# Kernel tuning notes

Measured on AMD Instinct MI355X. Metric: run time of the kernel, lower is better.

Reference implementation:

```python
import jax, jax.numpy as jnp
import numpy as np
from jax import lax

SIGMAS = (15.0, 80.0, 250.0)
DETAIL_WEIGHT = 0.0
ILLUM_WEIGHT = 1.0
EPS = 0.001


def _gaussian_kernel1d(sigma: float) -> np.ndarray:
    ks = int(2 * round(3 * sigma) + 1)
    if ks % 2 == 0:
        ks += 1
    x = np.arange(ks, dtype=np.float32) - (ks - 1) / 2.0
    k = np.exp(-0.5 * (x / sigma) ** 2)
    return (k / k.sum()).astype(np.float32)


def _gaussian_blur(img: jnp.ndarray, sigma: float) -> jnp.ndarray:
    # Separable Gaussian blur with reflect padding (kornia gaussian_blur2d semantics).
    k = jnp.asarray(_gaussian_kernel1d(sigma))
    ks = k.shape[0]
    p = ks // 2
    C = img.shape[1]
    dn = ('NCHW', 'OIHW', 'NCHW')
    kv = jnp.broadcast_to(k.reshape(1, 1, ks, 1), (C, 1, ks, 1))  # vertical pass
    kh = jnp.broadcast_to(k.reshape(1, 1, 1, ks), (C, 1, 1, ks))  # horizontal pass
    x = jnp.pad(img, ((0, 0), (0, 0), (p, p), (0, 0)), mode='reflect')
    x = lax.conv_general_dilated(x, kv, (1, 1), 'VALID', dimension_numbers=dn,
                                 feature_group_count=C)
    x = jnp.pad(x, ((0, 0), (0, 0), (0, 0), (p, p)), mode='reflect')
    x = lax.conv_general_dilated(x, kh, (1, 1), 'VALID', dimension_numbers=dn,
                                 feature_group_count=C)
    return x


def _multi_scale_retinex(input_img: jnp.ndarray) -> jnp.ndarray:
    img = jnp.clip(input_img, EPS, 1.0)
    log_img = jnp.log(img)
    acc = jnp.zeros_like(log_img)
    for sigma in SIGMAS:
        blur = jnp.maximum(_gaussian_blur(img, sigma), EPS)
        acc = acc + (log_img - jnp.log(blur))
    return acc / len(SIGMAS)


def setup_inputs() -> dict:
    key = jax.random.key(0)
    input_img = jax.random.uniform(key, (2, 3, 1024, 1024), dtype=jnp.float32)
    return {"input_img": input_img}


def reference(input_img):
    reflectance = _multi_scale_retinex(input_img)
    gx = reflectance[:, :, :, :-1] - reflectance[:, :, :, 1:]
    gy = reflectance[:, :, :-1, :] - reflectance[:, :, 1:, :]
    loss_detail = jnp.abs(gx).mean() + jnp.abs(gy).mean()
    illumination = jnp.log(jnp.maximum(input_img, EPS)) - reflectance
    igx = illumination[:, :, :, :-1] - illumination[:, :, :, 1:]
    igy = illumination[:, :, :-1, :] - illumination[:, :, 1:, :]
    loss_smooth_illum = jnp.abs(igx).mean() + jnp.abs(igy).mean()
    loss = DETAIL_WEIGHT * loss_detail + ILLUM_WEIGHT * loss_smooth_illum
    return (loss, loss_detail, loss_smooth_illum, reflectance, illumination)
```

## Files before the change

### kernel.cpp

```cpp
#include <hip/hip_runtime.h>
#include <math.h>

#define IMN 1024
#define IMGSZ (IMN * IMN)
#define NIMG 6
#define EPSV 0.001f
#define NB1 4096

typedef unsigned short u16;
typedef _Float16 f16;
typedef __attribute__((ext_vector_type(8))) _Float16 half8;
typedef __attribute__((ext_vector_type(16))) float floatx16;

__device__ __forceinline__ u16 f16_bits(float v) {
  union { f16 h; u16 b; } u;
  u.h = (f16)v;
  return u.b;
}

__global__ __launch_bounds__(256) void build_taps_k(float* __restrict__ taps) {
  const int kss[3] = {91, 481, 1501};
  const float sig[3] = {15.f, 80.f, 250.f};
  int s = blockIdx.x;
  int ks = kss[s];
  float sigma = sig[s];
  float* t = taps + s * 1536;
  float ctr = (float)(ks - 1) * 0.5f;
  __shared__ float red[256];
  float loc = 0.f;
  for (int i = threadIdx.x; i < ks; i += 256) {
    float x = ((float)i - ctr) / sigma;
    float v = expf(-0.5f * x * x);
    t[i] = v;
    loc += v;
  }
  red[threadIdx.x] = loc;
  __syncthreads();
  for (int o = 128; o > 0; o >>= 1) {
    if (threadIdx.x < o) red[threadIdx.x] += red[threadIdx.x + o];
    __syncthreads();
  }
  float inv = 1.f / red[0];
  for (int i = threadIdx.x; i < ks; i += 256) t[i] *= inv;
}

__global__ __launch_bounds__(256) void build_w_k(const float* __restrict__ taps, int ks,
                                                 u16* __restrict__ WFr) {
  int r = blockIdx.x;
  int p = ks >> 1;
  __shared__ float row[IMN];
  for (int i = threadIdx.x; i < IMN; i += 256) row[i] = 0.f;
  __syncthreads();
  for (int t = threadIdx.x; t < ks; t += 256) {
    int q = r + t - p;
    int j = q < 0 ? -q : (q > IMN - 1 ? 2 * (IMN - 1) - q : q);
    atomicAdd(&row[j], taps[t]);
  }
  __syncthreads();
  for (int i = threadIdx.x; i < IMN; i += 256)
    WFr[r * IMN + i] = f16_bits(row[i] * 256.f);
}

__global__ __launch_bounds__(256) void split_img_k(const float* __restrict__ inp,
                                                   u16* __restrict__ H) {
  int i4 = (blockIdx.x * 256 + threadIdx.x) * 4;
  float4 v = *(const float4*)&inp[i4];
  float x[4] = {v.x, v.y, v.z, v.w};
  u16 h[4];
#pragma unroll
  for (int e = 0; e < 4; e++) h[e] = f16_bits(fminf(fmaxf(x[e], EPSV), 1.f));
  *(uint2*)&H[i4] = make_uint2((unsigned)h[0] | ((unsigned)h[1] << 16),
                               (unsigned)h[2] | ((unsigned)h[3] << 16));
}

template <int EPI>
__global__ __launch_bounds__(256, 4) void gemm_pass(
    const u16* __restrict__ AH, const u16* __restrict__ WF,
    u16* __restrict__ OH, float* __restrict__ OF, int sBase, int outByZ, int rmw) {
  __shared__ u16 smem[2 * 128 * 32 + 256];
  u16* Af = smem;
  u16* Bf = smem + 128 * 32;
  int z = blockIdx.z;
  int zs = z / 6;
  int s = (gridDim.z >= 18) ? (sBase + 2 - zs) : (sBase + zs);
  int i = z - zs * 6;
  const u16* Ag = AH + (size_t)(EPI == 0 ? i : z) * IMGSZ;
  const u16* Bg = WF + (size_t)s * IMGSZ;
  int bm = blockIdx.y * 128, bn = blockIdx.x * 128;
  int tid = threadIdx.x;
  int lane = tid & 63, w = tid >> 6;
  int wm = (w >> 1) * 64, wn = (w & 1) * 64;
  int lrow = lane & 31, lh = lane >> 5;
  int sig = (lrow >> 1) & 3;
  int tr = tid >> 2;
  int tc = (tid & 3) * 8;
  int sslot = ((tid & 3) ^ ((tr >> 1) & 3)) * 8;
  floatx16 acc[2][2] = {};

  int p = (s == 0) ? 45 : (s == 1) ? 240 : 750;
  int klo = bn - p;
  klo = (klo < 0 ? 0 : klo) & ~31;
  int khi = bn + 128 + p;
  if (khi > IMN) khi = IMN;

  for (int k0 = klo; k0 < khi; k0 += 32) {
    uint4 a0 = *(const uint4*)&Ag[(size_t)(bm + tr) * IMN + k0 + tc];
    uint4 a1 = *(const uint4*)&Ag[(size_t)(bm + tr + 64) * IMN + k0 + tc];
    uint4 b0 = *(const uint4*)&Bg[(size_t)(bn + tr) * IMN + k0 + tc];
    uint4 b1 = *(const uint4*)&Bg[(size_t)(bn + tr + 64) * IMN + k0 + tc];
    *(uint4*)&Af[tr * 32 + sslot] = a0;
    *(uint4*)&Af[(tr + 64) * 32 + sslot] = a1;
    *(uint4*)&Bf[tr * 32 + sslot] = b0;
    *(uint4*)&Bf[(tr + 64) * 32 + sslot] = b1;
    __syncthreads();
#pragma unroll
    for (int kk = 0; kk < 32; kk += 16) {
      int sl = (kk >> 3) + lh;
      int so = ((sl ^ sig) * 8);
      half8 ah[2], bh[2];
#pragma unroll
      for (int mt = 0; mt < 2; mt++)
        ah[mt] = *(const half8*)&Af[(wm + mt * 32 + lrow) * 32 + so];
#pragma unroll
      for (int nt2 = 0; nt2 < 2; nt2++)
        bh[nt2] = *(const half8*)&Bf[(wn + nt2 * 32 + lrow) * 32 + so];
#pragma unroll
      for (int mt = 0; mt < 2; mt++)
#pragma unroll
        for (int nt2 = 0; nt2 < 2; nt2++)
          acc[mt][nt2] = __builtin_amdgcn_mfma_f32_32x32x16_f16(ah[mt], bh[nt2], acc[mt][nt2], 0, 0, 0);
    }
    __syncthreads();
  }

  float* lf = (float*)smem + w * 1056;
#pragma unroll
  for (int mt = 0; mt < 2; mt++)
#pragma unroll
    for (int nt = 0; nt < 2; nt++) {
#pragma unroll
      for (int rq = 0; rq < 4; rq++)
#pragma unroll
        for (int e = 0; e < 4; e++)
          lf[lrow * 33 + rq * 8 + lh * 4 + e] = acc[mt][nt][rq * 4 + e];
      __syncthreads();
#pragma unroll
      for (int p4 = 0; p4 < 4; p4++) {
        int rl = p4 * 8 + (lane >> 3);
        int cl = (lane & 7) * 4;
        float v0 = lf[rl * 33 + cl + 0];
        float v1 = lf[rl * 33 + cl + 1];
        float v2 = lf[rl * 33 + cl + 2];
        float v3 = lf[rl * 33 + cl + 3];
        int gn = bn + wn + nt * 32 + rl;
        int gm = bm + wm + mt * 32 + cl;
        if (EPI == 0) {
          size_t go = (size_t)z * IMGSZ + (size_t)gn * IMN + gm;
          *(uint2*)&OH[go] = make_uint2(
              (unsigned)f16_bits(v0) | ((unsigned)f16_bits(v1) << 16),
              (unsigned)f16_bits(v2) | ((unsigned)f16_bits(v3) << 16));
        } else {
          const float us = 0x1p-16f;
          size_t go = (size_t)(outByZ ? z : i) * IMGSZ + (size_t)gn * IMN + gm;
          float4 rr = make_float4(logf(fmaxf(v0 * us, EPSV)), logf(fmaxf(v1 * us, EPSV)),
                                  logf(fmaxf(v2 * us, EPSV)), logf(fmaxf(v3 * us, EPSV)));
          if (rmw) {
            float4 pa = *(const float4*)&OF[go];
            rr.x += pa.x; rr.y += pa.y; rr.z += pa.z; rr.w += pa.w;
          }
          *(float4*)&OF[go] = rr;
        }
      }
      __syncthreads();
    }
}

__global__ __launch_bounds__(256) void loss_stage1_k(const float* __restrict__ inp,
                                                     const float* __restrict__ lb, int three,
                                                     float* __restrict__ refl,
                                                     float* __restrict__ illum,
                                                     float* __restrict__ pd,
                                                     float* __restrict__ ps) {
  const int stride = NB1 * 256;
  const int S = NIMG * IMGSZ;
  float sd = 0.f, ss = 0.f;
  for (int i = blockIdx.x * 256 + threadIdx.x; i < S; i += stride) {
    int c = i & (IMN - 1);
    int rr = (i >> 10) & (IMN - 1);
    float a0 = lb[i];
    if (three) a0 += lb[i + S] + lb[i + 2 * S];
    float I0 = a0 * (1.f / 3.f);
    float R0 = logf(fmaxf(inp[i], EPSV)) - I0;
    refl[i] = R0;
    illum[i] = I0;
    if (c < IMN - 1) {
      float a1 = lb[i + 1];
      if (three) a1 += lb[i + 1 + S] + lb[i + 1 + 2 * S];
      float I1 = a1 * (1.f / 3.f);
      float R1 = logf(fmaxf(inp[i + 1], EPSV)) - I1;
      sd += fabsf(R0 - R1);
      ss += fabsf(I0 - I1);
    }
    if (rr < IMN - 1) {
      float a2 = lb[i + IMN];
      if (three) a2 += lb[i + IMN + S] + lb[i + IMN + 2 * S];
      float I2 = a2 * (1.f / 3.f);
      float R2 = logf(fmaxf(inp[i + IMN], EPSV)) - I2;
      sd += fabsf(R0 - R2);
      ss += fabsf(I0 - I2);
    }
  }
  for (int o = 32; o > 0; o >>= 1) {
    sd += __shfl_down(sd, o);
    ss += __shfl_down(ss, o);
  }
  __shared__ float rsd[4], rss[4];
  int lane = threadIdx.x & 63, w = threadIdx.x >> 6;
  if (lane == 0) { rsd[w] = sd; rss[w] = ss; }
  __syncthreads();
  if (threadIdx.x == 0) {
    pd[blockIdx.x] = rsd[0] + rsd[1] + rsd[2] + rsd[3];
    ps[blockIdx.x] = rss[0] + rss[1] + rss[2] + rss[3];
  }
}

__global__ __launch_bounds__(256) void loss_stage2_k(const float* __restrict__ pd,
                                                     const float* __restrict__ ps,
                                                     float* __restrict__ out) {
  float sd = 0.f, ss = 0.f;
  for (int i = threadIdx.x; i < NB1; i += 256) {
    sd += pd[i];
    ss += ps[i];
  }
  for (int o = 32; o > 0; o >>= 1) {
    sd += __shfl_down(sd, o);
    ss += __shfl_down(ss, o);
  }
  __shared__ float rsd[4], rss[4];
  int lane = threadIdx.x & 63, w = threadIdx.x >> 6;
  if (lane == 0) { rsd[w] = sd; rss[w] = ss; }
  __syncthreads();
  if (threadIdx.x == 0) {
    float tsd = rsd[0] + rsd[1] + rsd[2] + rsd[3];
    float tss = rss[0] + rss[1] + rss[2] + rss[3];
    const float sc = 1.f / 6285312.f;
    out[0] = tss * sc;
    out[1] = tsd * sc;
    out[2] = tss * sc;
  }
}

extern "C" void kernel_launch(void* const* d_in, const int* in_sizes, int n_in,
                              void* d_out, int out_size, void* d_ws, size_t ws_size,
                              hipStream_t stream) {
  const float* inp = (const float*)d_in[0];
  float* out = (float*)d_out;
  float* refl = out + 3;
  float* illum = refl + (size_t)NIMG * IMGSZ;
  const int kss[3] = {91, 481, 1501};

  char* p = (char*)d_ws;
  float* taps = (float*)p;                  p += 32768;
  u16* WF = (u16*)p;                        p += (size_t)3 * IMGSZ * 2;
  u16* imgF = (u16*)p;                      p += (size_t)NIMG * IMGSZ * 2;
  size_t fixed = (size_t)(p - (char*)d_ws);
  size_t needT1 = fixed + (size_t)18 * IMGSZ * 2 + (size_t)18 * IMGSZ * 4;
  bool t1 = ws_size >= needT1;
  int nz = t1 ? 18 : 6;
  u16* UtH = (u16*)p;                       p += (size_t)nz * IMGSZ * 2;
  float* LB = (float*)p;
  float* pd = taps;
  float* ps = taps + NB1;

  build_taps_k<<<3, 256, 0, stream>>>(taps);
  for (int s = 0; s < 3; s++)
    build_w_k<<<IMN, 256, 0, stream>>>(taps + s * 1536, kss[s], WF + (size_t)s * IMGSZ);
  split_img_k<<<NIMG * IMGSZ / 1024, 256, 0, stream>>>(inp, imgF);

  if (t1) {
    dim3 g(8, 8, 18);
    gemm_pass<0><<<g, 256, 0, stream>>>(imgF, WF, UtH, nullptr, 0, 1, 0);
    gemm_pass<1><<<g, 256, 0, stream>>>(UtH, WF, nullptr, LB, 0, 1, 0);
  } else {
    dim3 g(8, 8, 6);
    for (int s = 0; s < 3; s++) {
      gemm_pass<0><<<g, 256, 0, stream>>>(imgF, WF, UtH, nullptr, s, 0, 0);
      gemm_pass<1><<<g, 256, 0, stream>>>(UtH, WF, nullptr, LB, s, 0, s > 0);
    }
  }
  loss_stage1_k<<<NB1, 256, 0, stream>>>(inp, LB, t1 ? 1 : 0, refl, illum, pd, ps);
  loss_stage2_k<<<1, 256, 0, stream>>>(pd, ps, out);
}
```

Measured before the change: 254.4 us.

## Use single-wave 64x64 GEMM tiles with double-buffered direct global-to-LDS loads

The banded blur GEMM moves from 256-thread blocks with 128x128 tiles to 64-thread single-wavefront blocks with 64x64 tiles. Loads now use global_load_lds into two LDS buffers and are pipelined with explicit vmcnt waits, so the next K-slab is prefetched while MFMAs run and block barriers are no longer needed. Smaller tiles fit the band of the small-sigma kernels more tightly and launch four times as many blocks. In exchange, each operand is reloaded more often because per-block reuse drops, and correctness now depends on the hand-written waitcnt ordering.

```diff
diff --git a/kernel.cpp b/kernel.cpp
--- a/kernel.cpp
+++ b/kernel.cpp
@@ -11,11 +11,17 @@
 typedef _Float16 f16;
 typedef __attribute__((ext_vector_type(8))) _Float16 half8;
 typedef __attribute__((ext_vector_type(16))) float floatx16;
+typedef __attribute__((address_space(1))) const unsigned gu32;
+typedef __attribute__((address_space(3))) unsigned lu32;
 
 __device__ __forceinline__ u16 f16_bits(float v) {
   union { f16 h; u16 b; } u;
   u.h = (f16)v;
   return u.b;
+}
+
+__device__ __forceinline__ void dma16(const u16* g, u16* l) {
+  __builtin_amdgcn_global_load_lds((gu32*)g, (lu32*)l, 16, 0, 0);
 }
 
 __global__ __launch_bounds__(256) void build_taps_k(float* __restrict__ taps) {
@@ -74,76 +80,90 @@
 }
 
 template <int EPI>
-__global__ __launch_bounds__(256, 4) void gemm_pass(
+__global__ __launch_bounds__(64) void gemm_pass(
     const u16* __restrict__ AH, const u16* __restrict__ WF,
     u16* __restrict__ OH, float* __restrict__ OF, int sBase, int outByZ, int rmw) {
-  __shared__ u16 smem[2 * 128 * 32 + 256];
-  u16* Af = smem;
-  u16* Bf = smem + 128 * 32;
+  __shared__ u16 smem[2 * 2 * 64 * 32 + 32];
   int z = blockIdx.z;
   int zs = z / 6;
   int s = (gridDim.z >= 18) ? (sBase + 2 - zs) : (sBase + zs);
   int i = z - zs * 6;
   const u16* Ag = AH + (size_t)(EPI == 0 ? i : z) * IMGSZ;
   const u16* Bg = WF + (size_t)s * IMGSZ;
-  int bm = blockIdx.y * 128, bn = blockIdx.x * 128;
-  int tid = threadIdx.x;
-  int lane = tid & 63, w = tid >> 6;
-  int wm = (w >> 1) * 64, wn = (w & 1) * 64;
+  int bm = blockIdx.y * 64, bn = blockIdx.x * 64;
+  int lane = threadIdx.x;
   int lrow = lane & 31, lh = lane >> 5;
   int sig = (lrow >> 1) & 3;
-  int tr = tid >> 2;
-  int tc = (tid & 3) * 8;
-  int sslot = ((tid & 3) ^ ((tr >> 1) & 3)) * 8;
+  int csw = ((lane & 3) ^ ((lane >> 3) & 3)) * 8;
+  int r4 = lane >> 2;
   floatx16 acc[2][2] = {};
 
   int p = (s == 0) ? 45 : (s == 1) ? 240 : 750;
   int klo = bn - p;
   klo = (klo < 0 ? 0 : klo) & ~31;
-  int khi = bn + 128 + p;
+  int khi = bn + 64 + p;
   if (khi > IMN) khi = IMN;
-
-  for (int k0 = klo; k0 < khi; k0 += 32) {
-    uint4 a0 = *(const uint4*)&Ag[(size_t)(bm + tr) * IMN + k0 + tc];
-    uint4 a1 = *(const uint4*)&Ag[(size_t)(bm + tr + 64) * IMN + k0 + tc];
-    uint4 b0 = *(const uint4*)&Bg[(size_t)(bn + tr) * IMN + k0 + tc];
-    uint4 b1 = *(const uint4*)&Bg[(size_t)(bn + tr + 64) * IMN + k0 + tc];
-    *(uint4*)&Af[tr * 32 + sslot] = a0;
-    *(uint4*)&Af[(tr + 64) * 32 + sslot] = a1;
-    *(uint4*)&Bf[tr * 32 + sslot] = b0;
-    *(uint4*)&Bf[(tr + 64) * 32 + sslot] = b1;
-    __syncthreads();
+  int ntl = (khi - klo + 31) >> 5;
+
+  const u16* ga[4];
+  const u16* gb[4];
+#pragma unroll
+  for (int j = 0; j < 4; j++) {
+    ga[j] = Ag + (size_t)(bm + j * 16 + r4) * IMN + csw;
+    gb[j] = Bg + (size_t)(bn + j * 16 + r4) * IMN + csw;
+  }
+  u16* buf0 = smem;
+  u16* buf1 = smem + 4096;
+
+#pragma unroll
+  for (int j = 0; j < 4; j++) {
+    dma16(ga[j] + klo, buf0 + j * 512);
+    dma16(gb[j] + klo, buf0 + 2048 + j * 512);
+  }
+  asm volatile("s_waitcnt vmcnt(0)" ::: "memory");
+
+  for (int t = 0; t < ntl; t++) {
+    u16* cb = (t & 1) ? buf1 : buf0;
+    if (t + 1 < ntl) {
+      u16* nb = (t & 1) ? buf0 : buf1;
+      int k1 = klo + (t + 1) * 32;
+#pragma unroll
+      for (int j = 0; j < 4; j++) {
+        dma16(ga[j] + k1, nb + j * 512);
+        dma16(gb[j] + k1, nb + 2048 + j * 512);
+      }
+      asm volatile("s_waitcnt vmcnt(8)" ::: "memory");
+    } else {
+      asm volatile("s_waitcnt vmcnt(0)" ::: "memory");
+    }
 #pragma unroll
     for (int kk = 0; kk < 32; kk += 16) {
-      int sl = (kk >> 3) + lh;
-      int so = ((sl ^ sig) * 8);
+      int so = ((((kk >> 3) + lh) ^ sig) * 8);
       half8 ah[2], bh[2];
 #pragma unroll
       for (int mt = 0; mt < 2; mt++)
-        ah[mt] = *(const half8*)&Af[(wm + mt * 32 + lrow) * 32 + so];
-#pragma unroll
-      for (int nt2 = 0; nt2 < 2; nt2++)
-        bh[nt2] = *(const half8*)&Bf[(wn + nt2 * 32 + lrow) * 32 + so];
+        ah[mt] = *(const half8*)&cb[(mt * 32 + lrow) * 32 + so];
+#pragma unroll
+      for (int nn = 0; nn < 2; nn++)
+        bh[nn] = *(const half8*)&cb[2048 + (nn * 32 + lrow) * 32 + so];
 #pragma unroll
       for (int mt = 0; mt < 2; mt++)
 #pragma unroll
-        for (int nt2 = 0; nt2 < 2; nt2++)
-          acc[mt][nt2] = __builtin_amdgcn_mfma_f32_32x32x16_f16(ah[mt], bh[nt2], acc[mt][nt2], 0, 0, 0);
-    }
-    __syncthreads();
-  }
-
-  float* lf = (float*)smem + w * 1056;
+        for (int nn = 0; nn < 2; nn++)
+          acc[mt][nn] = __builtin_amdgcn_mfma_f32_32x32x16_f16(ah[mt], bh[nn], acc[mt][nn], 0, 0, 0);
+    }
+  }
+
+  float* lf = (float*)smem;
 #pragma unroll
   for (int mt = 0; mt < 2; mt++)
 #pragma unroll
-    for (int nt = 0; nt < 2; nt++) {
+    for (int nn = 0; nn < 2; nn++) {
 #pragma unroll
       for (int rq = 0; rq < 4; rq++)
 #pragma unroll
         for (int e = 0; e < 4; e++)
-          lf[lrow * 33 + rq * 8 + lh * 4 + e] = acc[mt][nt][rq * 4 + e];
-      __syncthreads();
+          lf[lrow * 33 + rq * 8 + lh * 4 + e] = acc[mt][nn][rq * 4 + e];
 #pragma unroll
       for (int p4 = 0; p4 < 4; p4++) {
         int rl = p4 * 8 + (lane >> 3);
@@ -152,8 +172,8 @@
         float v1 = lf[rl * 33 + cl + 1];
         float v2 = lf[rl * 33 + cl + 2];
         float v3 = lf[rl * 33 + cl + 3];
-        int gn = bn + wn + nt * 32 + rl;
-        int gm = bm + wm + mt * 32 + cl;
+        int gn = bn + nn * 32 + rl;
+        int gm = bm + mt * 32 + cl;
         if (EPI == 0) {
           size_t go = (size_t)z * IMGSZ + (size_t)gn * IMN + gm;
           *(uint2*)&OH[go] = make_uint2(
@@ -171,7 +191,6 @@
           *(float4*)&OF[go] = rr;
         }
       }
-      __syncthreads();
     }
 }
 
@@ -278,14 +297,14 @@
   split_img_k<<<NIMG * IMGSZ / 1024, 256, 0, stream>>>(inp, imgF);
 
   if (t1) {
-    dim3 g(8, 8, 18);
-    gemm_pass<0><<<g, 256, 0, stream>>>(imgF, WF, UtH, nullptr, 0, 1, 0);
-    gemm_pass<1><<<g, 256, 0, stream>>>(UtH, WF, nullptr, LB, 0, 1, 0);
+    dim3 g(16, 16, 18);
+    gemm_pass<0><<<g, 64, 0, stream>>>(imgF, WF, UtH, nullptr, 0, 1, 0);
+    gemm_pass<1><<<g, 64, 0, stream>>>(UtH, WF, nullptr, LB, 0, 1, 0);
   } else {
-    dim3 g(8, 8, 6);
+    dim3 g(16, 16, 6);
     for (int s = 0; s < 3; s++) {
-      gemm_pass<0><<<g, 256, 0, stream>>>(imgF, WF, UtH, nullptr, s, 0, 0);
-      gemm_pass<1><<<g, 256, 0, stream>>>(UtH, WF, nullptr, LB, s, 0, s > 0);
+      gemm_pass<0><<<g, 64, 0, stream>>>(imgF, WF, UtH, nullptr, s, 0, 0);
+      gemm_pass<1><<<g, 64, 0, stream>>>(UtH, WF, nullptr, LB, s, 0, s > 0);
     }
   }
   loss_stage1_k<<<NB1, 256, 0, stream>>>(inp, LB, t1 ? 1 : 0, refl, illum, pd, ps);
```

Result: no change. 259.1 us (+1.8%).

## Store log-blur intermediates in fp16 and vectorize loss stage to four pixels

Applied to the files above, without the earlier changes.

The per-scale log-blur buffer written by the second GEMM pass and read by the loss kernel changes from fp32 to fp16, halving its traffic and workspace footprint, which also lowers the threshold for the single 18-slice launch path. The loss stage now handles four consecutive pixels per thread with vector loads of fp16 and float4 input, reusing horizontal neighbours instead of reloading them per pixel. The cost is reduced precision in the stored log-blur values, which carries into the reflectance and illumination outputs and the gradient sums.

```diff
diff --git a/kernel.cpp b/kernel.cpp
--- a/kernel.cpp
+++ b/kernel.cpp
@@ -16,6 +16,17 @@
   union { f16 h; u16 b; } u;
   u.h = (f16)v;
   return u.b;
+}
+__device__ __forceinline__ float f16_val(u16 b) {
+  union { f16 h; u16 b2; } u;
+  u.b2 = b;
+  return (float)u.h;
+}
+__device__ __forceinline__ void unp4(uint2 v, float* o) {
+  o[0] = f16_val((u16)(v.x & 0xffff));
+  o[1] = f16_val((u16)(v.x >> 16));
+  o[2] = f16_val((u16)(v.y & 0xffff));
+  o[3] = f16_val((u16)(v.y >> 16));
 }
 
 __global__ __launch_bounds__(256) void build_taps_k(float* __restrict__ taps) {
@@ -76,7 +87,7 @@
 template <int EPI>
 __global__ __launch_bounds__(256, 4) void gemm_pass(
     const u16* __restrict__ AH, const u16* __restrict__ WF,
-    u16* __restrict__ OH, float* __restrict__ OF, int sBase, int outByZ, int rmw) {
+    u16* __restrict__ OH, u16* __restrict__ LB16, int sBase, int outByZ, int rmw) {
   __shared__ u16 smem[2 * 128 * 32 + 256];
   u16* Af = smem;
   u16* Bf = smem + 128 * 32;
@@ -162,13 +173,19 @@
         } else {
           const float us = 0x1p-16f;
           size_t go = (size_t)(outByZ ? z : i) * IMGSZ + (size_t)gn * IMN + gm;
-          float4 rr = make_float4(logf(fmaxf(v0 * us, EPSV)), logf(fmaxf(v1 * us, EPSV)),
-                                  logf(fmaxf(v2 * us, EPSV)), logf(fmaxf(v3 * us, EPSV)));
+          float r0 = logf(fmaxf(v0 * us, EPSV));
+          float r1 = logf(fmaxf(v1 * us, EPSV));
+          float r2 = logf(fmaxf(v2 * us, EPSV));
+          float r3 = logf(fmaxf(v3 * us, EPSV));
           if (rmw) {
-            float4 pa = *(const float4*)&OF[go];
-            rr.x += pa.x; rr.y += pa.y; rr.z += pa.z; rr.w += pa.w;
+            uint2 pa = *(const uint2*)&LB16[go];
+            float o4[4];
+            unp4(pa, o4);
+            r0 += o4[0]; r1 += o4[1]; r2 += o4[2]; r3 += o4[3];
           }
-          *(float4*)&OF[go] = rr;
+          *(uint2*)&LB16[go] = make_uint2(
+              (unsigned)f16_bits(r0) | ((unsigned)f16_bits(r1) << 16),
+              (unsigned)f16_bits(r2) | ((unsigned)f16_bits(r3) << 16));
         }
       }
       __syncthreads();
@@ -176,38 +193,83 @@
 }
 
 __global__ __launch_bounds__(256) void loss_stage1_k(const float* __restrict__ inp,
-                                                     const float* __restrict__ lb, int three,
+                                                     const u16* __restrict__ lb, int three,
                                                      float* __restrict__ refl,
                                                      float* __restrict__ illum,
                                                      float* __restrict__ pd,
                                                      float* __restrict__ ps) {
+  const int S = NIMG * IMGSZ;
+  const int NCH = S >> 2;
   const int stride = NB1 * 256;
-  const int S = NIMG * IMGSZ;
+  const float third = 1.f / 3.f;
   float sd = 0.f, ss = 0.f;
-  for (int i = blockIdx.x * 256 + threadIdx.x; i < S; i += stride) {
-    int c = i & (IMN - 1);
-    int rr = (i >> 10) & (IMN - 1);
-    float a0 = lb[i];
-    if (three) a0 += lb[i + S] + lb[i + 2 * S];
-    float I0 = a0 * (1.f / 3.f);
-    float R0 = logf(fmaxf(inp[i], EPSV)) - I0;
-    refl[i] = R0;
-    illum[i] = I0;
-    if (c < IMN - 1) {
-      float a1 = lb[i + 1];
-      if (three) a1 += lb[i + 1 + S] + lb[i + 1 + 2 * S];
-      float I1 = a1 * (1.f / 3.f);
-      float R1 = logf(fmaxf(inp[i + 1], EPSV)) - I1;
-      sd += fabsf(R0 - R1);
-      ss += fabsf(I0 - I1);
-    }
-    if (rr < IMN - 1) {
-      float a2 = lb[i + IMN];
-      if (three) a2 += lb[i + IMN + S] + lb[i + IMN + 2 * S];
-      float I2 = a2 * (1.f / 3.f);
-      float R2 = logf(fmaxf(inp[i + IMN], EPSV)) - I2;
-      sd += fabsf(R0 - R2);
-      ss += fabsf(I0 - I2);
+  for (int c = blockIdx.x * 256 + threadIdx.x; c < NCH; c += stride) {
+    int i = c << 2;
+    int col = i & (IMN - 1);
+    int row = (i >> 10) & (IMN - 1);
+    bool hR = col < (IMN - 4);
+    bool hD = row < (IMN - 1);
+    float sum[5];
+    {
+      float t0[4];
+      unp4(*(const uint2*)&lb[i], t0);
+      sum[0] = t0[0]; sum[1] = t0[1]; sum[2] = t0[2]; sum[3] = t0[3];
+      sum[4] = hR ? f16_val(lb[i + 4]) : 0.f;
+      if (three) {
+        float t1[4], t2[4];
+        unp4(*(const uint2*)&lb[i + S], t1);
+        unp4(*(const uint2*)&lb[i + 2 * S], t2);
+#pragma unroll
+        for (int j = 0; j < 4; j++) sum[j] += t1[j] + t2[j];
+        if (hR) sum[4] += f16_val(lb[i + 4 + S]) + f16_val(lb[i + 4 + 2 * S]);
+      }
+    }
+    float Iv[5], Rv[5];
+#pragma unroll
+    for (int j = 0; j < 5; j++) Iv[j] = sum[j] * third;
+    float4 xv = *(const float4*)&inp[i];
+    float xs[4] = {xv.x, xv.y, xv.z, xv.w};
+#pragma unroll
+    for (int j = 0; j < 4; j++) Rv[j] = logf(fmaxf(xs[j], EPSV)) - Iv[j];
+    if (hR) Rv[4] = logf(fmaxf(inp[i + 4], EPSV)) - Iv[4];
+#pragma unroll
+    for (int j = 0; j < 4; j++) {
+      refl[i + j] = Rv[j];
+      illum[i + j] = Iv[j];
+    }
+#pragma unroll
+    for (int j = 0; j < 3; j++) {
+      sd += fabsf(Rv[j] - Rv[j + 1]);
+      ss += fabsf(Iv[j] - Iv[j + 1]);
+    }
+    if (hR) {
+      sd += fabsf(Rv[3] - Rv[4]);
+      ss += fabsf(Iv[3] - Iv[4]);
+    }
+    if (hD) {
+      int ib = i + IMN;
+      float sb[4];
+      {
+        float t0[4];
+        unp4(*(const uint2*)&lb[ib], t0);
+        sb[0] = t0[0]; sb[1] = t0[1]; sb[2] = t0[2]; sb[3] = t0[3];
+        if (three) {
+          float t1[4], t2[4];
+          unp4(*(const uint2*)&lb[ib + S], t1);
+          unp4(*(const uint2*)&lb[ib + 2 * S], t2);
+#pragma unroll
+          for (int j = 0; j < 4; j++) sb[j] += t1[j] + t2[j];
+        }
+      }
+      float4 xb = *(const float4*)&inp[ib];
+      float xbs[4] = {xb.x, xb.y, xb.z, xb.w};
+#pragma unroll
+      for (int j = 0; j < 4; j++) {
+        float Ib = sb[j] * third;
+        float Rb = logf(fmaxf(xbs[j], EPSV)) - Ib;
+        sd += fabsf(Rv[j] - Rb);
+        ss += fabsf(Iv[j] - Ib);
+      }
     }
   }
   for (int o = 32; o > 0; o >>= 1) {
@@ -264,11 +326,11 @@
   u16* WF = (u16*)p;                        p += (size_t)3 * IMGSZ * 2;
   u16* imgF = (u16*)p;                      p += (size_t)NIMG * IMGSZ * 2;
   size_t fixed = (size_t)(p - (char*)d_ws);
-  size_t needT1 = fixed + (size_t)18 * IMGSZ * 2 + (size_t)18 * IMGSZ * 4;
+  size_t needT1 = fixed + (size_t)18 * IMGSZ * 2 + (size_t)18 * IMGSZ * 2;
   bool t1 = ws_size >= needT1;
   int nz = t1 ? 18 : 6;
   u16* UtH = (u16*)p;                       p += (size_t)nz * IMGSZ * 2;
-  float* LB = (float*)p;
+  u16* LB = (u16*)p;
   float* pd = taps;
   float* ps = taps + NB1;
 
```

After: 238.0 us. -6.5%, faster.
